# Performance work log

Measured on AMD Instinct MI355X. Metric: run time of the kernel, lower is better.

## Reference

```python
import jax
import jax.numpy as jnp
import numpy as np
from jax import lax

DELTA = float(np.exp(-2.0))  # rule-creation density threshold


def codebook_lamb(x):
    """Online growing RBF prototype codebook (ALMMo-style) for one layer.

    x: [N, M]. Returns lamb: [N] normalized density of each sample at its
    assigned rule. Faithful (corrected) semantics of Layer.__call__:
      - SEN = squared L2 norm per sample (over feature dim)
      - global mean / mean squared norm over the batch
      - sequential per-sample: if max RBF density over existing rules < exp(-2),
        append a new rule (prototype=c=x, SENc=||x||^2, support=1);
        else update rule_star. Note the source's `support[rule_star] = +1`
        assigns 1, so the running mean update degenerates to c[rule_star]=x,
        SENc[rule_star]=||x||^2 -- replicated here.
      - distances use the (never-updated) prototypes; bandwidth stau uses c.
    """
    N, M = x.shape
    SENx = jnp.sum(x * x, axis=-1)                      # [N]
    gmean = jnp.mean(x, axis=0)                         # [M]
    base = jnp.mean(SENx) - jnp.sum(gmean * gmean)      # SENgmean - SEN(gmean)
    R = N                                               # worst case: one rule/sample

    protos0 = jnp.zeros((R, M), x.dtype)
    pn20 = jnp.zeros((R,), x.dtype)                     # ||proto_r||^2 (carried)
    c0 = jnp.zeros((R, M), x.dtype)
    cn20 = jnp.zeros((R,), x.dtype)                     # ||c_r||^2 (carried)
    SENc0 = jnp.zeros((R,), x.dtype)
    count0 = jnp.int32(0)

    ridx = jnp.arange(R)

    def step(carry, inp):
        protos, pn2, c, cn2, SENc, count = carry
        xi, sxi = inp                                   # [M], scalar
        valid = ridx < count
        stau = (base + SENc - cn2) * 0.5                # [R]
        dist = sxi + pn2 - 2.0 * (protos @ xi)          # [R] ||xi - proto_r||^2
        dens = jnp.where(valid, jnp.exp(-dist / stau), -jnp.inf)
        idx = jnp.argmax(dens)
        vmax = dens[idx]
        new = (count == 0) | (vmax < DELTA)
        slot = jnp.where(new, count, idx)
        # both branches set c/SENc at slot to xi/sxi (support resets to 1)
        c = c.at[slot].set(xi)
        cn2 = cn2.at[slot].set(sxi)
        SENc = SENc.at[slot].set(sxi)
        # only a new rule writes a prototype (OOB scatter when count==R is dropped)
        protos = protos.at[count].set(jnp.where(new, xi, protos[count]))
        pn2 = pn2.at[count].set(jnp.where(new, sxi, pn2[count]))
        count = count + new.astype(count.dtype)
        return (protos, pn2, c, cn2, SENc, count), slot

    (protos, pn2, c, cn2, SENc, count), rules = lax.scan(
        step, (protos0, pn20, c0, cn20, SENc0, count0), (x, SENx)
    )

    # final densities of all samples under all (valid) rules: [R, N]
    stau = (base + SENc - cn2) * 0.5                    # [R]
    dist = SENx[None, :] + pn2[:, None] - 2.0 * (protos @ x.T)
    dens = jnp.where((ridx < count)[:, None], jnp.exp(-dist / stau[:, None]), 0.0)
    dens_xn = dens[rules, jnp.arange(N)]                # density at assigned rule
    lamb = dens_xn / jnp.sum(dens, axis=0)              # normalize over rules
    return lamb


def setup_inputs() -> dict:
    key = jax.random.key(0)
    k = jax.random.split(key, 5)
    N, D_IN, D_H, D_OUT = 2048, 2048, 2048, 1024
    s0 = 1.0 / np.sqrt(D_IN)
    s1 = 1.0 / np.sqrt(D_H)
    return {
        "x": jax.random.normal(k[0], (N, D_IN), jnp.float32),
        "W0": jax.random.normal(k[1], (D_H, D_IN), jnp.float32) * s0,
        "b0": jax.random.normal(k[2], (D_H,), jnp.float32) * s0,
        "W1": jax.random.normal(k[3], (D_OUT, D_H), jnp.float32) * s1,
        "b1": jax.random.normal(k[4], (D_OUT,), jnp.float32) * s1,
    }


def reference(x, W0, b0, W1, b1):
    lambs = []
    h = x
    for W, b in ((W0, b0), (W1, b1)):
        lambs.append(codebook_lamb(h))          # per-layer codebook on layer input
        h = jax.nn.sigmoid(h @ W.T + b)         # torch.nn.Linear + sigmoid
    return h, jnp.stack(lambs)                  # ([N, d_out], [n_layers, N])
```

## Files before the change

### kernel.cpp

```cpp
#include <hip/hip_runtime.h>
#include <cstdint>
#include <cstddef>


#define DELTA_F 0.13533528323661270f
#define MBYTE (1u << 20)

typedef __bf16 bf16;
typedef bf16 bf16x8 __attribute__((ext_vector_type(8)));
typedef bf16 bf16x4 __attribute__((ext_vector_type(4)));
typedef float f32x4 __attribute__((ext_vector_type(4)));

typedef __attribute__((address_space(1))) void as1_void;
typedef __attribute__((address_space(3))) void as3_void;

__device__ __forceinline__ void gload16(const bf16* g, bf16* l) {
  __builtin_amdgcn_global_load_lds((as1_void*)g, (as3_void*)l, 16, 0, 0);
}

template <bool SIG_B16>
__global__ __launch_bounds__(512, 4) void gemm_fused(
    const bf16* __restrict__ A, const bf16* __restrict__ Bm,
    float* __restrict__ G, bf16* __restrict__ Hb, float* __restrict__ Fo,
    const float* __restrict__ bias, float* __restrict__ SEN,
    float* __restrict__ sumAll, int K, int sigW) {
  __shared__ __align__(16) char smem[32768];
  const int tid = threadIdx.x;
  const int wave = tid >> 6, lane = tid & 63;
  const int quad = lane >> 4, l16 = lane & 15;
  const int kg = wave & 1, wm = (wave >> 1) & 1, wn = (wave >> 2) & 1;
  const int m0 = blockIdx.y * 128, n0 = blockIdx.x * 128;
  const int waveM = wm * 64, waveN = wn * 64;
  const bool isGram = (n0 < 2048);
  const int sr8 = lane >> 3, slot = lane & 7;
  const int gk = (slot ^ sr8) * 8;
  const bf16* aSrc = A + (size_t)(m0 + wave * 16 + sr8) * K + gk;
  const bf16* bSrc = Bm + (size_t)(n0 + wave * 16 + sr8) * K + gk;
  char* const aDst = smem + wave * 2048;
  char* const bDst = smem + 16384 + wave * 2048;
  const int swz = ((kg * 4 + quad) ^ (l16 & 7)) * 16;
  const int aOff = (waveM + l16) * 128 + swz;
  const int bOff = 16384 + (waveN + l16) * 128 + swz;

  f32x4 acc[4][4] = {};

  for (int k0 = 0; k0 < K; k0 += 64) {
    gload16(aSrc + k0, (bf16*)aDst);
    gload16(aSrc + 8 * (size_t)K + k0, (bf16*)(aDst + 1024));
    gload16(bSrc + k0, (bf16*)bDst);
    gload16(bSrc + 8 * (size_t)K + k0, (bf16*)(bDst + 1024));
    __syncthreads();
    bf16x8 af[4], bfr[4];
#pragma unroll
    for (int i = 0; i < 4; ++i) af[i] = *(const bf16x8*)(smem + aOff + i * 2048);
#pragma unroll
    for (int j = 0; j < 4; ++j) bfr[j] = *(const bf16x8*)(smem + bOff + j * 2048);
#pragma unroll
    for (int i = 0; i < 4; ++i)
#pragma unroll
      for (int j = 0; j < 4; ++j)
        acc[i][j] = __builtin_amdgcn_mfma_f32_16x16x32_bf16(af[i], bfr[j], acc[i][j], 0, 0, 0);
    __syncthreads();
  }

  float gsum = 0.f;
  char* const ex = smem + (wn * 2 + wm) * 8192;
#pragma unroll
  for (int round = 0; round < 2; ++round) {
    __syncthreads();
    if (kg == 1) {
#pragma unroll
      for (int ii = 0; ii < 2; ++ii)
#pragma unroll
        for (int j = 0; j < 4; ++j)
          *(f32x4*)(ex + (ii * 4 + j) * 1024 + lane * 16) = acc[round * 2 + ii][j];
    }
    __syncthreads();
    if (kg == 0) {
#pragma unroll
      for (int ii = 0; ii < 2; ++ii) {
        const int i = round * 2 + ii;
#pragma unroll
        for (int j = 0; j < 4; ++j) {
          f32x4 v = acc[i][j] + *(const f32x4*)(ex + (ii * 4 + j) * 1024 + lane * 16);
          const int col = n0 + waveN + j * 16 + l16;
          const float bv = isGram ? 0.f : bias[col - 2048];
#pragma unroll
          for (int r = 0; r < 4; ++r) {
            const int row = m0 + waveM + i * 16 + quad * 4 + r;
            if (isGram) {
              const float val = v[r];
              G[(size_t)row * 2048 + col] = val;
              gsum += val;
              if (row == col) SEN[row] = val;
            } else {
              const float hv = 1.0f / (1.0f + expf(-(v[r] + bv)));
              const int c2 = col - 2048;
              if (SIG_B16) Hb[(size_t)row * 2048 + c2] = (bf16)hv;
              else Fo[(size_t)row * sigW + c2] = hv;
            }
          }
        }
      }
    }
  }
  if (isGram && kg == 0) {
    for (int off = 32; off > 0; off >>= 1) gsum += __shfl_down(gsum, off, 64);
    if (lane == 0) atomicAdd(sumAll, gsum);
  }
}

__device__ __forceinline__ float block_reduce_sum(float s, float* ws4) {
  for (int off = 32; off > 0; off >>= 1) s += __shfl_down(s, off, 64);
  const int tid = threadIdx.x;
  if ((tid & 63) == 0) ws4[tid >> 6] = s;
  __syncthreads();
  return ws4[0] + ws4[1] + ws4[2] + ws4[3];
}

__global__ void f2b_all(const float* __restrict__ x, const float* __restrict__ W0,
                        const float* __restrict__ W1, bf16* __restrict__ xb,
                        bf16* __restrict__ wb0, bf16* __restrict__ wb1,
                        float* __restrict__ scal) {
  const int idx = (blockIdx.x * 256 + threadIdx.x) * 4;
  if (blockIdx.x == 0 && threadIdx.x < 16) scal[threadIdx.x] = 0.f;
  const float* src;
  bf16* dst;
  int off;
  if (idx < 4194304) { src = x; dst = xb; off = idx; }
  else if (idx < 8388608) { src = W0; dst = wb0; off = idx - 4194304; }
  else { src = W1; dst = wb1; off = idx - 8388608; }
  f32x4 v = *(const f32x4*)(src + off);
  bf16x4 o;
  o.x = (bf16)v.x; o.y = (bf16)v.y; o.z = (bf16)v.z; o.w = (bf16)v.w;
  *(bf16x4*)(dst + off) = o;
}

__global__ void stau_kernel(const float* __restrict__ SEN, float* __restrict__ base,
                            int Nsamp) {
  const int tid = threadIdx.x;
  float s = 0.f;
  for (int i = tid; i < Nsamp; i += 256) s += SEN[i];
  __shared__ float ws4[4];
  const float tot = block_reduce_sum(s, ws4);
  if (tid == 0) {
    const float invN = 1.0f / (float)Nsamp;
    const float stau = 0.5f * (tot * invN - base[2] * invN * invN);
    base[0] = stau;
    base[1] = -1.0f / stau;
  }
}

__global__ void edgesum_kernel(const float* __restrict__ G, const float* __restrict__ SEN,
                               const float* __restrict__ base, int N,
                               int* __restrict__ e, float* __restrict__ S) {
  const int i = blockIdx.x, tid = threadIdx.x;
  const float ninv = base[1];
  const float si = SEN[i];
  const float* gi = G + (size_t)i * N;
  __shared__ int sflag;
  if (tid == 0) sflag = 0;
  __syncthreads();
  float s = 0.f;
  int f = 0;
  for (int j = tid; j < N; j += 256) {
    const float dens = expf((si + SEN[j] - 2.0f * gi[j]) * ninv);
    s += dens;
    if (j < i && dens >= DELTA_F) f = 1;
  }
  if (f) atomicOr(&sflag, 1);
  __shared__ float ws4[4];
  const float tot = block_reduce_sum(s, ws4);
  __syncthreads();
  if (tid == 0) { e[i] = sflag; S[i] = tot; }
}

__global__ void decide_kernel(const int* __restrict__ e, const float* __restrict__ G,
                              const float* __restrict__ SEN, const float* __restrict__ base,
                              int N, int* __restrict__ newflag, int* __restrict__ assigned,
                              int* __restrict__ rcnt, int* __restrict__ rlist) {
  __shared__ int s_flag[2048];
  __shared__ short s_list[2048];
  __shared__ short s_re[2048];
  __shared__ int s_T, s_reN;
  __shared__ int scan[256];
  __shared__ float rbest[256];
  __shared__ int rbj[256];
  const int tid = threadIdx.x;
  const float ninv = base[1];
  const int per = N / 256;
  int cnt = 0;
  for (int k = 0; k < per; ++k) {
    const int i = tid * per + k;
    const int ei = e[i];
    s_flag[i] = (ei == 0);
    if (ei == 0) { newflag[i] = 1; assigned[i] = i; }
    cnt += ei;
  }
  scan[tid] = cnt;
  if (tid == 0) s_reN = 0;
  __syncthreads();
  for (int off = 1; off < 256; off <<= 1) {
    const int v = scan[tid];
    const int add = (tid >= off) ? scan[tid - off] : 0;
    __syncthreads();
    scan[tid] = v + add;
    __syncthreads();
  }
  int pos = scan[tid] - cnt;
  for (int k = 0; k < per; ++k) {
    const int i = tid * per + k;
    if (!s_flag[i]) s_list[pos++] = (short)i;
  }
  if (tid == 255) s_T = scan[255];
  __syncthreads();
  const int T = s_T;
  for (int t = 0; t < T; ++t) {
    const int i = s_list[t];
    const float si = SEN[i];
    const float* gi = G + (size_t)i * N;
    float best = -1.0f;
    int bestj = 0x7fffffff;
    for (int j = tid; j < i; j += 256) {
      if (s_flag[j]) {
        const float dens = expf((si + SEN[j] - 2.0f * gi[j]) * ninv);
        if (dens > best || (dens == best && j < bestj)) { best = dens; bestj = j; }
      }
    }
    rbest[tid] = best; rbj[tid] = bestj;
    __syncthreads();
    if (tid == 0) {
      float b = -1.0f;
      int bj = 0x7fffffff;
      for (int k = 0; k < 256; ++k)
        if (rbest[k] > b || (rbest[k] == b && rbj[k] < bj)) { b = rbest[k]; bj = rbj[k]; }
      if (b < DELTA_F) { s_flag[i] = 1; newflag[i] = 1; assigned[i] = i; }
      else { newflag[i] = 0; assigned[i] = bj; s_re[s_reN++] = (short)i; }
    }
    __syncthreads();
  }
  const int reN = s_reN;
  for (int t = tid; t < reN; t += 256) rlist[t] = s_re[t];
  if (tid == 0) rcnt[0] = reN;
}

__global__ void lamb_fix(const float* __restrict__ G, const float* __restrict__ SEN,
                         const float* __restrict__ base, const float* __restrict__ S,
                         const int* __restrict__ assigned, const int* __restrict__ rcnt,
                         const int* __restrict__ rlist, int N, float* __restrict__ lamb) {
  const int n = blockIdx.x * 256 + threadIdx.x;
  const float ninv = base[1];
  const float sn = SEN[n];
  const float* gn = G + (size_t)n * N;
  const int a = assigned[n];
  const float da = expf((sn + SEN[a] - 2.0f * gn[a]) * ninv);
  float denom = S[n];
  const int rc = rcnt[0];
  for (int t = 0; t < rc; ++t) {
    const int j = rlist[t];
    denom -= expf((sn + SEN[j] - 2.0f * gn[j]) * ninv);
  }
  lamb[n] = da / denom;
}

extern "C" void kernel_launch(void* const* d_in, const int* in_sizes, int n_in,
                              void* d_out, int out_size, void* d_ws, size_t ws_size,
                              hipStream_t stream) {
  const float* x = (const float*)d_in[0];
  const float* W0 = (const float*)d_in[1];
  const float* b0 = (const float*)d_in[2];
  const float* W1 = (const float*)d_in[3];
  const float* b1 = (const float*)d_in[4];
  float* out = (float*)d_out;

  const int N = 2048, DIN = 2048, DH = 2048, DOUT = 1024;

  char* w = (char*)d_ws;
  bf16* xb = (bf16*)(w);
  bf16* wb0 = (bf16*)(w + 8 * MBYTE);
  bf16* hb = (bf16*)(w + 16 * MBYTE);
  bf16* wb1 = (bf16*)(w + 24 * MBYTE);
  float* G = (float*)(w + 28 * MBYTE);
  float* SEN = (float*)(w + 44 * MBYTE);
  float* S = SEN + 2048;
  float* scal = S + 2048;
  int* e = (int*)(scal + 16);
  int* nf = e + 2048;
  int* as = nf + 2048;
  int* rcnt = as + 2048;
  int* rlist = rcnt + 16;

  float* lamb0 = out + (size_t)N * DOUT;
  float* lamb1 = lamb0 + N;

  f2b_all<<<10240, 256, 0, stream>>>(x, W0, W1, xb, wb0, wb1, scal);

  gemm_fused<true><<<dim3(32, 16), 512, 0, stream>>>(
      xb, xb, G, hb, nullptr, b0, SEN, scal + 2, DIN, DH);
  stau_kernel<<<1, 256, 0, stream>>>(SEN, scal + 0, N);
  edgesum_kernel<<<N, 256, 0, stream>>>(G, SEN, scal + 0, N, e, S);
  decide_kernel<<<1, 256, 0, stream>>>(e, G, SEN, scal + 0, N, nf, as, rcnt, rlist);
  lamb_fix<<<N / 256, 256, 0, stream>>>(G, SEN, scal + 0, S, as, rcnt, rlist, N, lamb0);

  gemm_fused<false><<<dim3(24, 16), 512, 0, stream>>>(
      hb, hb, G, nullptr, out, b1, SEN, scal + 6, DH, DOUT);
  stau_kernel<<<1, 256, 0, stream>>>(SEN, scal + 4, N);
  edgesum_kernel<<<N, 256, 0, stream>>>(G, SEN, scal + 4, N, e, S);
  decide_kernel<<<1, 256, 0, stream>>>(e, G, SEN, scal + 4, N, nf, as, rcnt, rlist);
  lamb_fix<<<N / 256, 256, 0, stream>>>(G, SEN, scal + 4, S, as, rcnt, rlist, N, lamb1);
}
```

Measured before the change: 231.6 us.

## Fuse each layer's pipeline into one cooperative megakernel with density epilogue

Each layer's work now runs in a single cooperative kernel, separated by grid-wide syncs, instead of separate conversion, stau, edgesum, decide and lamb kernels. The fp32 Gram matrix is no longer stored; the GEMM epilogue computes RBF densities directly, accumulates row sums and sets rule-creation flags with atomics. Squared norms and the column mean are now taken exactly from the inputs rather than from the Gram diagonal. The GEMM drops in-block split-K, using 256-thread blocks with a 32-wide K step. The aim is to cut launch overhead, the Gram round-trip and repeated exp work in the serial decide and lamb stages, at the cost of grid-sync overhead and a full grid co-residency requirement.

```diff
diff --git a/kernel.cpp b/kernel.cpp
--- a/kernel.cpp
+++ b/kernel.cpp
@@ -1,6 +1,9 @@
 #include <hip/hip_runtime.h>
+#include <hip/hip_cooperative_groups.h>
 #include <cstdint>
 #include <cstddef>
+
+namespace cg = cooperative_groups;
 
 
 #define DELTA_F 0.13533528323661270f
@@ -18,249 +21,310 @@
   __builtin_amdgcn_global_load_lds((as1_void*)g, (as3_void*)l, 16, 0, 0);
 }
 
-template <bool SIG_B16>
-__global__ __launch_bounds__(512, 4) void gemm_fused(
-    const bf16* __restrict__ A, const bf16* __restrict__ Bm,
-    float* __restrict__ G, bf16* __restrict__ Hb, float* __restrict__ Fo,
-    const float* __restrict__ bias, float* __restrict__ SEN,
-    float* __restrict__ sumAll, int K, int sigW) {
-  __shared__ __align__(16) char smem[32768];
+__device__ __forceinline__ float wave_reduce(float s) {
+  for (int o = 32; o > 0; o >>= 1) s += __shfl_down(s, o, 64);
+  return s;
+}
+
+struct MegaArgs {
+  const float* xf;
+  const bf16* hsrc;
+  const float* Wf;
+  const float* bias;
+  bf16* Ab;
+  bf16* Wb;
+  float* Dens;
+  bf16* Hb;
+  float* Fo;
+  float* SEN;
+  float* cpart;
+  float* scal;
+  float* S;
+  int* e;
+  int* as;
+  int* rcnt;
+  int* rlist;
+  float* lamb;
+};
+
+template <bool IS_L0>
+__global__ __launch_bounds__(256, 2) void mega(MegaArgs a) {
+  __shared__ __align__(16) char smem[16384];
+  cg::grid_group grid = cg::this_grid();
   const int tid = threadIdx.x;
   const int wave = tid >> 6, lane = tid & 63;
-  const int quad = lane >> 4, l16 = lane & 15;
-  const int kg = wave & 1, wm = (wave >> 1) & 1, wn = (wave >> 2) & 1;
-  const int m0 = blockIdx.y * 128, n0 = blockIdx.x * 128;
-  const int waveM = wm * 64, waveN = wn * 64;
-  const bool isGram = (n0 < 2048);
-  const int sr8 = lane >> 3, slot = lane & 7;
-  const int gk = (slot ^ sr8) * 8;
-  const bf16* aSrc = A + (size_t)(m0 + wave * 16 + sr8) * K + gk;
-  const bf16* bSrc = Bm + (size_t)(n0 + wave * 16 + sr8) * K + gk;
-  char* const aDst = smem + wave * 2048;
-  char* const bDst = smem + 16384 + wave * 2048;
-  const int swz = ((kg * 4 + quad) ^ (l16 & 7)) * 16;
-  const int aOff = (waveM + l16) * 128 + swz;
-  const int bOff = 16384 + (waveN + l16) * 128 + swz;
-
-  f32x4 acc[4][4] = {};
-
-  for (int k0 = 0; k0 < K; k0 += 64) {
-    gload16(aSrc + k0, (bf16*)aDst);
-    gload16(aSrc + 8 * (size_t)K + k0, (bf16*)(aDst + 1024));
-    gload16(bSrc + k0, (bf16*)bDst);
-    gload16(bSrc + 8 * (size_t)K + k0, (bf16*)(bDst + 1024));
+  const int lb = blockIdx.y * gridDim.x + blockIdx.x;
+
+  if (IS_L0) {
+    if (lb < 256) {
+#pragma unroll
+      for (int rr = 0; rr < 2; ++rr) {
+        const int row = lb * 8 + wave * 2 + rr;
+        const float* src = a.xf + (size_t)row * 2048;
+        bf16* dst = a.Ab + (size_t)row * 2048;
+        float ss = 0.f;
+        for (int c = lane * 4; c < 2048; c += 256) {
+          f32x4 v = *(const f32x4*)(src + c);
+          bf16x4 o;
+          o.x = (bf16)v.x; o.y = (bf16)v.y; o.z = (bf16)v.z; o.w = (bf16)v.w;
+          *(bf16x4*)(dst + c) = o;
+          ss += v.x * v.x + v.y * v.y + v.z * v.z + v.w * v.w;
+        }
+        ss = wave_reduce(ss);
+        if (lane == 0) a.SEN[row] = ss;
+      }
+    } else if (lb < 384) {
+      const int b = lb - 256, rc = b >> 3, cc = b & 7;
+      const int col = cc * 256 + tid;
+      const float* p = a.xf + (size_t)rc * 128 * 2048 + col;
+      float s = 0.f;
+      for (int r = 0; r < 128; ++r) s += p[(size_t)r * 2048];
+      a.cpart[(size_t)rc * 2048 + col] = s;
+    } else {
+      const int b = lb - 384;
+      const float* src = a.Wf + (size_t)b * 32768;
+      bf16* dst = a.Wb + (size_t)b * 32768;
+      for (int c = tid * 4; c < 32768; c += 1024) {
+        f32x4 v = *(const f32x4*)(src + c);
+        bf16x4 o;
+        o.x = (bf16)v.x; o.y = (bf16)v.y; o.z = (bf16)v.z; o.w = (bf16)v.w;
+        *(bf16x4*)(dst + c) = o;
+      }
+      if (b == 0)
+        for (int i = tid; i < 2048; i += 256) { a.S[i] = 0.f; a.e[i] = 0; }
+    }
+  } else {
+    if (lb < 128) {
+#pragma unroll
+      for (int rr = 0; rr < 4; ++rr) {
+        const int row = lb * 16 + wave * 4 + rr;
+        const bf16* src = a.hsrc + (size_t)row * 2048;
+        float ss = 0.f;
+        for (int c = lane * 8; c < 2048; c += 512) {
+          bf16x8 v8 = *(const bf16x8*)(src + c);
+#pragma unroll
+          for (int q = 0; q < 8; ++q) { const float f = (float)v8[q]; ss += f * f; }
+        }
+        ss = wave_reduce(ss);
+        if (lane == 0) a.SEN[row] = ss;
+      }
+    } else if (lb < 256) {
+      const int b = lb - 128, rc = b >> 3, cc = b & 7;
+      const int col = cc * 256 + tid;
+      const bf16* p = a.hsrc + (size_t)rc * 128 * 2048 + col;
+      float s = 0.f;
+      for (int r = 0; r < 128; ++r) s += (float)p[(size_t)r * 2048];
+      a.cpart[(size_t)rc * 2048 + col] = s;
+    } else {
+      const int b = lb - 256;
+      const float* src = a.Wf + (size_t)b * 16384;
+      bf16* dst = a.Wb + (size_t)b * 16384;
+      for (int c = tid * 4; c < 16384; c += 1024) {
+        f32x4 v = *(const f32x4*)(src + c);
+        bf16x4 o;
+        o.x = (bf16)v.x; o.y = (bf16)v.y; o.z = (bf16)v.z; o.w = (bf16)v.w;
+        *(bf16x4*)(dst + c) = o;
+      }
+      if (b == 0)
+        for (int i = tid; i < 2048; i += 256) { a.S[i] = 0.f; a.e[i] = 0; }
+    }
+  }
+  grid.sync();
+
+  if (lb == 0) {
+    float ssen = 0.f;
+    for (int i = tid; i < 2048; i += 256) ssen += a.SEN[i];
+    float sg2 = 0.f;
+    for (int c = tid; c < 2048; c += 256) {
+      float cs = 0.f;
+#pragma unroll
+      for (int p = 0; p < 16; ++p) cs += a.cpart[(size_t)p * 2048 + c];
+      const float gm = cs * (1.f / 2048.f);
+      sg2 += gm * gm;
+    }
+    float* r1 = (float*)smem;
+    float* r2 = r1 + 256;
+    r1[tid] = ssen; r2[tid] = sg2;
     __syncthreads();
-    bf16x8 af[4], bfr[4];
-#pragma unroll
-    for (int i = 0; i < 4; ++i) af[i] = *(const bf16x8*)(smem + aOff + i * 2048);
-#pragma unroll
-    for (int j = 0; j < 4; ++j) bfr[j] = *(const bf16x8*)(smem + bOff + j * 2048);
-#pragma unroll
-    for (int i = 0; i < 4; ++i)
-#pragma unroll
-      for (int j = 0; j < 4; ++j)
-        acc[i][j] = __builtin_amdgcn_mfma_f32_16x16x32_bf16(af[i], bfr[j], acc[i][j], 0, 0, 0);
+    for (int s = 128; s; s >>= 1) {
+      if (tid < s) { r1[tid] += r1[tid + s]; r2[tid] += r2[tid + s]; }
+      __syncthreads();
+    }
+    if (tid == 0) {
+      const float stau = 0.5f * (r1[0] * (1.f / 2048.f) - r2[0]);
+      a.scal[0] = stau;
+      a.scal[1] = -1.f / stau;
+    }
+  }
+  grid.sync();
+
+  {
+    const float ninv = a.scal[1];
+    const int quad = lane >> 4, l16 = lane & 15;
+    const int wm = wave & 1, wn = wave >> 1;
+    const int m0 = blockIdx.y * 128, n0 = blockIdx.x * 128;
+    const int waveM = wm * 64, waveN = wn * 64;
+    const bool isGram = (blockIdx.x < 16);
+    const int sr = lane >> 2, slot = lane & 3;
+    const int gk = (slot ^ (sr & 3)) * 8;
+    const bf16* aSrc = a.Ab + (size_t)(m0 + wave * 32 + sr) * 2048 + gk;
+    const bf16* bSrc = a.Ab + (size_t)(n0 + wave * 32 + sr) * 2048 + gk;
+    bf16* const aDst0 = (bf16*)(smem + wave * 2048);
+    bf16* const aDst1 = (bf16*)(smem + wave * 2048 + 1024);
+    bf16* const bDst0 = (bf16*)(smem + 8192 + wave * 2048);
+    bf16* const bDst1 = (bf16*)(smem + 8192 + wave * 2048 + 1024);
+    const int rdA = (waveM + l16) * 64 + (quad ^ (l16 & 3)) * 16;
+    const int rdB = 8192 + (waveN + l16) * 64 + (quad ^ (l16 & 3)) * 16;
+
+    f32x4 acc[4][4] = {};
+    for (int k0 = 0; k0 < 2048; k0 += 32) {
+      gload16(aSrc + k0, aDst0);
+      gload16(aSrc + 16 * 2048 + k0, aDst1);
+      gload16(bSrc + k0, bDst0);
+      gload16(bSrc + 16 * 2048 + k0, bDst1);
+      __syncthreads();
+      bf16x8 af[4], bfr[4];
+#pragma unroll
+      for (int i = 0; i < 4; ++i) af[i] = *(const bf16x8*)(smem + rdA + i * 1024);
+#pragma unroll
+      for (int j = 0; j < 4; ++j) bfr[j] = *(const bf16x8*)(smem + rdB + j * 1024);
+#pragma unroll
+      for (int i = 0; i < 4; ++i)
+#pragma unroll
+        for (int j = 0; j < 4; ++j)
+          acc[i][j] = __builtin_amdgcn_mfma_f32_16x16x32_bf16(af[i], bfr[j], acc[i][j], 0, 0, 0);
+      __syncthreads();
+    }
+
+    if (isGram) {
+#pragma unroll
+      for (int i = 0; i < 4; ++i) {
+        const int rbase = m0 + waveM + i * 16 + quad * 4;
+        const f32x4 si4 = *(const f32x4*)(a.SEN + rbase);
+        float rp[4] = {0.f, 0.f, 0.f, 0.f};
+        int er = 0;
+#pragma unroll
+        for (int j = 0; j < 4; ++j) {
+          const int col = n0 + waveN + j * 16 + l16;
+          const float sj = a.SEN[col];
+#pragma unroll
+          for (int r = 0; r < 4; ++r) {
+            const float dens = __expf((si4[r] + sj - 2.0f * acc[i][j][r]) * ninv);
+            a.Dens[(size_t)(rbase + r) * 2048 + col] = dens;
+            rp[r] += dens;
+            if (col < rbase + r && dens >= DELTA_F) er |= (1 << r);
+          }
+        }
+#pragma unroll
+        for (int r = 0; r < 4; ++r) {
+          float v = rp[r];
+          v += __shfl_xor(v, 1, 64); v += __shfl_xor(v, 2, 64);
+          v += __shfl_xor(v, 4, 64); v += __shfl_xor(v, 8, 64);
+          if (l16 == 0) atomicAdd(a.S + rbase + r, v);
+        }
+        int ef = er;
+        ef |= __shfl_xor(ef, 1, 64); ef |= __shfl_xor(ef, 2, 64);
+        ef |= __shfl_xor(ef, 4, 64); ef |= __shfl_xor(ef, 8, 64);
+        if (l16 == 0 && ef) {
+#pragma unroll
+          for (int r = 0; r < 4; ++r)
+            if (ef & (1 << r)) atomicOr(a.e + rbase + r, 1);
+        }
+      }
+    } else {
+#pragma unroll
+      for (int i = 0; i < 4; ++i) {
+        const int rbase = m0 + waveM + i * 16 + quad * 4;
+#pragma unroll
+        for (int j = 0; j < 4; ++j) {
+          const int c2 = n0 - 2048 + waveN + j * 16 + l16;
+          const float bv = a.bias[c2];
+#pragma unroll
+          for (int r = 0; r < 4; ++r) {
+            const float hv = 1.0f / (1.0f + __expf(-(acc[i][j][r] + bv)));
+            if (IS_L0) a.Hb[(size_t)(rbase + r) * 2048 + c2] = (bf16)hv;
+            else a.Fo[(size_t)(rbase + r) * 1024 + c2] = hv;
+          }
+        }
+      }
+    }
+  }
+  grid.sync();
+
+  if (lb == 0) {
+    char* s_flag = smem;
+    short* s_list = (short*)(smem + 2048);
+    short* s_re = (short*)(smem + 6144);
+    int* scan = (int*)(smem + 10240);
+    float* rbest = (float*)(smem + 11264);
+    int* rbj = (int*)(smem + 12288);
+    int* s_T = (int*)(smem + 13312);
+    int* s_reN = (int*)(smem + 13316);
+    int cnt = 0;
+#pragma unroll
+    for (int k = 0; k < 8; ++k) {
+      const int i = tid * 8 + k;
+      const int ei = a.e[i];
+      s_flag[i] = (ei == 0);
+      if (ei == 0) a.as[i] = i;
+      cnt += ei;
+    }
+    scan[tid] = cnt;
+    if (tid == 0) s_reN[0] = 0;
     __syncthreads();
-  }
-
-  float gsum = 0.f;
-  char* const ex = smem + (wn * 2 + wm) * 8192;
-#pragma unroll
-  for (int round = 0; round < 2; ++round) {
+    for (int off = 1; off < 256; off <<= 1) {
+      const int v = scan[tid];
+      const int add = (tid >= off) ? scan[tid - off] : 0;
+      __syncthreads();
+      scan[tid] = v + add;
+      __syncthreads();
+    }
+    int pos = scan[tid] - cnt;
+#pragma unroll
+    for (int k = 0; k < 8; ++k) {
+      const int i = tid * 8 + k;
+      if (!s_flag[i]) s_list[pos++] = (short)i;
+    }
+    if (tid == 255) s_T[0] = scan[255];
     __syncthreads();
-    if (kg == 1) {
-#pragma unroll
-      for (int ii = 0; ii < 2; ++ii)
-#pragma unroll
-        for (int j = 0; j < 4; ++j)
-          *(f32x4*)(ex + (ii * 4 + j) * 1024 + lane * 16) = acc[round * 2 + ii][j];
-    }
-    __syncthreads();
-    if (kg == 0) {
-#pragma unroll
-      for (int ii = 0; ii < 2; ++ii) {
-        const int i = round * 2 + ii;
-#pragma unroll
-        for (int j = 0; j < 4; ++j) {
-          f32x4 v = acc[i][j] + *(const f32x4*)(ex + (ii * 4 + j) * 1024 + lane * 16);
-          const int col = n0 + waveN + j * 16 + l16;
-          const float bv = isGram ? 0.f : bias[col - 2048];
-#pragma unroll
-          for (int r = 0; r < 4; ++r) {
-            const int row = m0 + waveM + i * 16 + quad * 4 + r;
-            if (isGram) {
-              const float val = v[r];
-              G[(size_t)row * 2048 + col] = val;
-              gsum += val;
-              if (row == col) SEN[row] = val;
-            } else {
-              const float hv = 1.0f / (1.0f + expf(-(v[r] + bv)));
-              const int c2 = col - 2048;
-              if (SIG_B16) Hb[(size_t)row * 2048 + c2] = (bf16)hv;
-              else Fo[(size_t)row * sigW + c2] = hv;
-            }
-          }
-        }
-      }
-    }
-  }
-  if (isGram && kg == 0) {
-    for (int off = 32; off > 0; off >>= 1) gsum += __shfl_down(gsum, off, 64);
-    if (lane == 0) atomicAdd(sumAll, gsum);
-  }
-}
-
-__device__ __forceinline__ float block_reduce_sum(float s, float* ws4) {
-  for (int off = 32; off > 0; off >>= 1) s += __shfl_down(s, off, 64);
-  const int tid = threadIdx.x;
-  if ((tid & 63) == 0) ws4[tid >> 6] = s;
-  __syncthreads();
-  return ws4[0] + ws4[1] + ws4[2] + ws4[3];
-}
-
-__global__ void f2b_all(const float* __restrict__ x, const float* __restrict__ W0,
-                        const float* __restrict__ W1, bf16* __restrict__ xb,
-                        bf16* __restrict__ wb0, bf16* __restrict__ wb1,
-                        float* __restrict__ scal) {
-  const int idx = (blockIdx.x * 256 + threadIdx.x) * 4;
-  if (blockIdx.x == 0 && threadIdx.x < 16) scal[threadIdx.x] = 0.f;
-  const float* src;
-  bf16* dst;
-  int off;
-  if (idx < 4194304) { src = x; dst = xb; off = idx; }
-  else if (idx < 8388608) { src = W0; dst = wb0; off = idx - 4194304; }
-  else { src = W1; dst = wb1; off = idx - 8388608; }
-  f32x4 v = *(const f32x4*)(src + off);
-  bf16x4 o;
-  o.x = (bf16)v.x; o.y = (bf16)v.y; o.z = (bf16)v.z; o.w = (bf16)v.w;
-  *(bf16x4*)(dst + off) = o;
-}
-
-__global__ void stau_kernel(const float* __restrict__ SEN, float* __restrict__ base,
-                            int Nsamp) {
-  const int tid = threadIdx.x;
-  float s = 0.f;
-  for (int i = tid; i < Nsamp; i += 256) s += SEN[i];
-  __shared__ float ws4[4];
-  const float tot = block_reduce_sum(s, ws4);
-  if (tid == 0) {
-    const float invN = 1.0f / (float)Nsamp;
-    const float stau = 0.5f * (tot * invN - base[2] * invN * invN);
-    base[0] = stau;
-    base[1] = -1.0f / stau;
-  }
-}
-
-__global__ void edgesum_kernel(const float* __restrict__ G, const float* __restrict__ SEN,
-                               const float* __restrict__ base, int N,
-                               int* __restrict__ e, float* __restrict__ S) {
-  const int i = blockIdx.x, tid = threadIdx.x;
-  const float ninv = base[1];
-  const float si = SEN[i];
-  const float* gi = G + (size_t)i * N;
-  __shared__ int sflag;
-  if (tid == 0) sflag = 0;
-  __syncthreads();
-  float s = 0.f;
-  int f = 0;
-  for (int j = tid; j < N; j += 256) {
-    const float dens = expf((si + SEN[j] - 2.0f * gi[j]) * ninv);
-    s += dens;
-    if (j < i && dens >= DELTA_F) f = 1;
-  }
-  if (f) atomicOr(&sflag, 1);
-  __shared__ float ws4[4];
-  const float tot = block_reduce_sum(s, ws4);
-  __syncthreads();
-  if (tid == 0) { e[i] = sflag; S[i] = tot; }
-}
-
-__global__ void decide_kernel(const int* __restrict__ e, const float* __restrict__ G,
-                              const float* __restrict__ SEN, const float* __restrict__ base,
-                              int N, int* __restrict__ newflag, int* __restrict__ assigned,
-                              int* __restrict__ rcnt, int* __restrict__ rlist) {
-  __shared__ int s_flag[2048];
-  __shared__ short s_list[2048];
-  __shared__ short s_re[2048];
-  __shared__ int s_T, s_reN;
-  __shared__ int scan[256];
-  __shared__ float rbest[256];
-  __shared__ int rbj[256];
-  const int tid = threadIdx.x;
-  const float ninv = base[1];
-  const int per = N / 256;
-  int cnt = 0;
-  for (int k = 0; k < per; ++k) {
-    const int i = tid * per + k;
-    const int ei = e[i];
-    s_flag[i] = (ei == 0);
-    if (ei == 0) { newflag[i] = 1; assigned[i] = i; }
-    cnt += ei;
-  }
-  scan[tid] = cnt;
-  if (tid == 0) s_reN = 0;
-  __syncthreads();
-  for (int off = 1; off < 256; off <<= 1) {
-    const int v = scan[tid];
-    const int add = (tid >= off) ? scan[tid - off] : 0;
-    __syncthreads();
-    scan[tid] = v + add;
-    __syncthreads();
-  }
-  int pos = scan[tid] - cnt;
-  for (int k = 0; k < per; ++k) {
-    const int i = tid * per + k;
-    if (!s_flag[i]) s_list[pos++] = (short)i;
-  }
-  if (tid == 255) s_T = scan[255];
-  __syncthreads();
-  const int T = s_T;
-  for (int t = 0; t < T; ++t) {
-    const int i = s_list[t];
-    const float si = SEN[i];
-    const float* gi = G + (size_t)i * N;
-    float best = -1.0f;
-    int bestj = 0x7fffffff;
-    for (int j = tid; j < i; j += 256) {
-      if (s_flag[j]) {
-        const float dens = expf((si + SEN[j] - 2.0f * gi[j]) * ninv);
-        if (dens > best || (dens == best && j < bestj)) { best = dens; bestj = j; }
-      }
-    }
-    rbest[tid] = best; rbj[tid] = bestj;
-    __syncthreads();
-    if (tid == 0) {
-      float b = -1.0f;
-      int bj = 0x7fffffff;
-      for (int k = 0; k < 256; ++k)
-        if (rbest[k] > b || (rbest[k] == b && rbj[k] < bj)) { b = rbest[k]; bj = rbj[k]; }
-      if (b < DELTA_F) { s_flag[i] = 1; newflag[i] = 1; assigned[i] = i; }
-      else { newflag[i] = 0; assigned[i] = bj; s_re[s_reN++] = (short)i; }
-    }
-    __syncthreads();
-  }
-  const int reN = s_reN;
-  for (int t = tid; t < reN; t += 256) rlist[t] = s_re[t];
-  if (tid == 0) rcnt[0] = reN;
-}
-
-__global__ void lamb_fix(const float* __restrict__ G, const float* __restrict__ SEN,
-                         const float* __restrict__ base, const float* __restrict__ S,
-                         const int* __restrict__ assigned, const int* __restrict__ rcnt,
-                         const int* __restrict__ rlist, int N, float* __restrict__ lamb) {
-  const int n = blockIdx.x * 256 + threadIdx.x;
-  const float ninv = base[1];
-  const float sn = SEN[n];
-  const float* gn = G + (size_t)n * N;
-  const int a = assigned[n];
-  const float da = expf((sn + SEN[a] - 2.0f * gn[a]) * ninv);
-  float denom = S[n];
-  const int rc = rcnt[0];
-  for (int t = 0; t < rc; ++t) {
-    const int j = rlist[t];
-    denom -= expf((sn + SEN[j] - 2.0f * gn[j]) * ninv);
-  }
-  lamb[n] = da / denom;
+    const int T = s_T[0];
+    for (int t = 0; t < T; ++t) {
+      const int i = s_list[t];
+      const float* di = a.Dens + (size_t)i * 2048;
+      float best = -1.0f;
+      int bestj = 0x7fffffff;
+      for (int j = tid; j < i; j += 256) {
+        if (s_flag[j]) {
+          const float d = di[j];
+          if (d > best || (d == best && j < bestj)) { best = d; bestj = j; }
+        }
+      }
+      rbest[tid] = best; rbj[tid] = bestj;
+      __syncthreads();
+      if (tid == 0) {
+        float b = -1.0f;
+        int bj = 0x7fffffff;
+        for (int k = 0; k < 256; ++k)
+          if (rbest[k] > b || (rbest[k] == b && rbj[k] < bj)) { b = rbest[k]; bj = rbj[k]; }
+        if (b < DELTA_F) { s_flag[i] = 1; a.as[i] = i; }
+        else { a.as[i] = bj; s_re[s_reN[0]++] = (short)i; }
+      }
+      __syncthreads();
+    }
+    const int reN = s_reN[0];
+    for (int t = tid; t < reN; t += 256) a.rlist[t] = s_re[t];
+    if (tid == 0) a.rcnt[0] = reN;
+  }
+  grid.sync();
+
+  if (lb < 8) {
+    const int n = lb * 256 + tid;
+    const int aa = a.as[n];
+    float denom = a.S[n];
+    const int rc = a.rcnt[0];
+    for (int t = 0; t < rc; ++t) denom -= a.Dens[(size_t)n * 2048 + a.rlist[t]];
+    a.lamb[n] = a.Dens[(size_t)n * 2048 + aa] / denom;
+  }
 }
 
 extern "C" void kernel_launch(void* const* d_in, const int* in_sizes, int n_in,
@@ -273,39 +337,33 @@
   const float* b1 = (const float*)d_in[4];
   float* out = (float*)d_out;
 
-  const int N = 2048, DIN = 2048, DH = 2048, DOUT = 1024;
-
   char* w = (char*)d_ws;
   bf16* xb = (bf16*)(w);
   bf16* wb0 = (bf16*)(w + 8 * MBYTE);
   bf16* hb = (bf16*)(w + 16 * MBYTE);
   bf16* wb1 = (bf16*)(w + 24 * MBYTE);
-  float* G = (float*)(w + 28 * MBYTE);
+  float* Dens = (float*)(w + 28 * MBYTE);
   float* SEN = (float*)(w + 44 * MBYTE);
   float* S = SEN + 2048;
   float* scal = S + 2048;
   int* e = (int*)(scal + 16);
-  int* nf = e + 2048;
-  int* as = nf + 2048;
+  int* as = e + 2048;
   int* rcnt = as + 2048;
   int* rlist = rcnt + 16;
-
-  float* lamb0 = out + (size_t)N * DOUT;
-  float* lamb1 = lamb0 + N;
-
-  f2b_all<<<10240, 256, 0, stream>>>(x, W0, W1, xb, wb0, wb1, scal);
-
-  gemm_fused<true><<<dim3(32, 16), 512, 0, stream>>>(
-      xb, xb, G, hb, nullptr, b0, SEN, scal + 2, DIN, DH);
-  stau_kernel<<<1, 256, 0, stream>>>(SEN, scal + 0, N);
-  edgesum_kernel<<<N, 256, 0, stream>>>(G, SEN, scal + 0, N, e, S);
-  decide_kernel<<<1, 256, 0, stream>>>(e, G, SEN, scal + 0, N, nf, as, rcnt, rlist);
-  lamb_fix<<<N / 256, 256, 0, stream>>>(G, SEN, scal + 0, S, as, rcnt, rlist, N, lamb0);
-
-  gemm_fused<false><<<dim3(24, 16), 512, 0, stream>>>(
-      hb, hb, G, nullptr, out, b1, SEN, scal + 6, DH, DOUT);
-  stau_kernel<<<1, 256, 0, stream>>>(SEN, scal + 4, N);
-  edgesum_kernel<<<N, 256, 0, stream>>>(G, SEN, scal + 4, N, e, S);
-  decide_kernel<<<1, 256, 0, stream>>>(e, G, SEN, scal + 4, N, nf, as, rcnt, rlist);
-  lamb_fix<<<N / 256, 256, 0, stream>>>(G, SEN, scal + 4, S, as, rcnt, rlist, N, lamb1);
+  float* cpart = (float*)(rlist + 2048);
+
+  float* lamb0 = out + (size_t)2048 * 1024;
+  float* lamb1 = lamb0 + 2048;
+
+  MegaArgs a0 = { x, nullptr, W0, b0, xb, wb0, Dens, hb, nullptr,
+                  SEN, cpart, scal, S, e, as, rcnt, rlist, lamb0 };
+  void* p0[] = { &a0 };
+  hipLaunchCooperativeKernel((const void*)mega<true>, dim3(32, 16), dim3(256),
+                             p0, 0, stream);
+
+  MegaArgs a1 = { nullptr, hb, W1, b1, hb, wb1, Dens, nullptr, out,
+                  SEN, cpart, scal, S, e, as, rcnt, rlist, lamb1 };
+  void* p1[] = { &a1 };
+  hipLaunchCooperativeKernel((const void*)mega<false>, dim3(24, 16), dim3(256),
+                             p1, 0, stream);
 }
```

Measured after the change: 644.7 us. 2.78x slower.
